# Performance work log

Hardware: AMD Instinct MI355X
Metric: run time of the kernel (lower is better)

## Reference

```python
import jax, jax.numpy as jnp
import numpy as np

B, C, H, W = 8, 256, 64, 64
R = 8
CP = max(C // R, 3)  # C' = 32


def setup_inputs() -> dict:
    key = jax.random.key(0)
    ks = jax.random.split(key, 9)
    s_in = 1.0 / np.sqrt(C)
    s_cp = 1.0 / np.sqrt(CP)
    return {
        "x": jax.random.normal(ks[0], (B, C, H, W), dtype=jnp.float32),
        "Wq": jax.random.uniform(ks[1], (CP, C), minval=-s_in, maxval=s_in, dtype=jnp.float32),
        "bq": jax.random.uniform(ks[2], (CP,), minval=-s_in, maxval=s_in, dtype=jnp.float32),
        "Wk": jax.random.uniform(ks[3], (CP, C), minval=-s_in, maxval=s_in, dtype=jnp.float32),
        "bk": jax.random.uniform(ks[4], (CP,), minval=-s_in, maxval=s_in, dtype=jnp.float32),
        "Wv": jax.random.uniform(ks[5], (CP, C), minval=-s_in, maxval=s_in, dtype=jnp.float32),
        "bv": jax.random.uniform(ks[6], (CP,), minval=-s_in, maxval=s_in, dtype=jnp.float32),
        "Wb": jax.random.uniform(ks[7], (C, CP), minval=-s_cp, maxval=s_cp, dtype=jnp.float32),
        "bb": jax.random.uniform(ks[8], (C,), minval=-s_cp, maxval=s_cp, dtype=jnp.float32),
    }


def reference(x, Wq, bq, Wk, bk, Wv, bv, Wb, bb):
    b, c, h, w = x.shape
    n = h * w
    xf = x.reshape(b, c, n)  # [B, C, N]
    # 1x1 convs == channel-wise linear projections
    q = jnp.einsum('oc,bcn->bon', Wq, xf) + bq[None, :, None]  # [B, C', N]
    k = jnp.einsum('oc,bcn->bon', Wk, xf) + bk[None, :, None]
    v = jnp.einsum('oc,bcn->bon', Wv, xf) + bv[None, :, None]
    # attention: softmax(Q^T K) over last dim -> [B, N, N]
    attn = jax.nn.softmax(jnp.einsum('bon,bom->bnm', q, k), axis=-1)
    # out[b,c,i] = sum_j v[b,c,j] * attn[b,j,i]
    out = jnp.einsum('bcj,bji->bci', v, attn)  # [B, C', N]
    back = jnp.einsum('co,bon->bcn', Wb, out) + bb[None, :, None]  # [B, C, N]
    return back.reshape(b, c, h, w) + x
```

## Files before the change

kernel.cpp:

```cpp
#include <hip/hip_runtime.h>
#include <hip/hip_bf16.h>

#define NB 8
#define CC 256
#define CP 32
#define NN 4096

typedef __attribute__((ext_vector_type(8))) short short8;
typedef __attribute__((ext_vector_type(4))) float floatx4;
typedef __attribute__((ext_vector_type(4))) int intx4;

static __device__ __forceinline__ ushort bf16r(float f) {
    __hip_bfloat16 h = __float2bfloat16(f);
    return *reinterpret_cast<ushort*>(&h);
}
static __device__ __forceinline__ float bf2f(ushort u) {
    union { unsigned int i; float f; } x;
    x.i = ((unsigned int)u) << 16;
    return x.f;
}
static __device__ __forceinline__ short8 load_frag(const ushort* p) {
    intx4 v = *reinterpret_cast<const intx4*>(p);
    return *reinterpret_cast<short8*>(&v);
}
static __device__ __forceinline__ unsigned int pk2(float a, float b) {
    unsigned int ua = __float_as_uint(a) + 0x8000u;
    unsigned int ub = __float_as_uint(b) + 0x8000u;
    return (ua >> 16) | (ub & 0xFFFF0000u);
}

__global__ void prep_w(const float* __restrict__ Wq, const float* __restrict__ Wk,
                       const float* __restrict__ Wv, ushort* __restrict__ W96) {
    int r = blockIdx.x, c = threadIdx.x;
    const float* src = (r < 32) ? (Wq + r * CC) : ((r < 64) ? (Wk + (r - 32) * CC) : (Wv + (r - 64) * CC));
    W96[r * CC + c] = bf16r(src[c]);
}

__global__ __launch_bounds__(256) void proj_kernel(
    const float* __restrict__ x, const ushort* __restrict__ W96,
    const float* __restrict__ bq, const float* __restrict__ bk, const float* __restrict__ bv,
    ushort* __restrict__ Qt, ushort* __restrict__ Kt, ushort* __restrict__ Vt) {
    int b = blockIdx.x >> 6;
    int nt = blockIdx.x & 63;
    int w = threadIdx.x >> 6, lane = threadIdx.x & 63;
    int l15 = lane & 15, q = lane >> 4;
    int n = nt * 64 + w * 16 + l15;
    const float* xb = x + (size_t)b * CC * NN + n;

    floatx4 acc[6];
#pragma unroll
    for (int t = 0; t < 6; t++) acc[t] = (floatx4){0.f, 0.f, 0.f, 0.f};

#pragma unroll
    for (int ks = 0; ks < 8; ks++) {
        int cbase = ks * 32 + q * 8;
        float xv[8];
#pragma unroll
        for (int jj = 0; jj < 8; jj++) xv[jj] = xb[(size_t)(cbase + jj) * NN];
        short8 bfrag;
#pragma unroll
        for (int jj = 0; jj < 8; jj++) bfrag[jj] = (short)bf16r(xv[jj]);
#pragma unroll
        for (int ot = 0; ot < 6; ot++) {
            short8 afrag = load_frag(&W96[(size_t)(ot * 16 + l15) * CC + ks * 32 + q * 8]);
            acc[ot] = __builtin_amdgcn_mfma_f32_16x16x32_bf16(afrag, bfrag, acc[ot], 0, 0, 0);
        }
    }
#pragma unroll
    for (int ot = 0; ot < 6; ot++) {
        const float* bias = (ot < 2) ? bq : ((ot < 4) ? bk : bv);
        ushort* dst = (ot < 2) ? Qt : ((ot < 4) ? Kt : Vt);
        int o0 = (ot & 1) * 16 + q * 4;
        float4 b4 = *reinterpret_cast<const float4*>(bias + o0);
        ushort4 pk;
        pk.x = bf16r(acc[ot][0] + b4.x);
        pk.y = bf16r(acc[ot][1] + b4.y);
        pk.z = bf16r(acc[ot][2] + b4.z);
        pk.w = bf16r(acc[ot][3] + b4.w);
        *reinterpret_cast<ushort4*>(&dst[((size_t)b * NN + n) * CP + o0]) = pk;
    }
}

__global__ __launch_bounds__(256) void passA_kernel(
    const ushort* __restrict__ Qt, const ushort* __restrict__ Kt, float* __restrict__ Fp) {
    __shared__ ushort kst[256 * CP];
    int bid = blockIdx.x;
    int mq = bid & 3;
    int jt = (bid >> 2) & 63;
    int b = bid >> 8;
    int w = threadIdx.x >> 6, lane = threadIdx.x & 63;
    int l15 = lane & 15, q = lane >> 4;
    int j = jt * 64 + w * 16 + l15;

    short8 af = load_frag(&Qt[((size_t)b * NN + j) * CP + q * 8]);
    floatx4 lacc = (floatx4){0.f, 0.f, 0.f, 0.f};

    for (int mc = 0; mc < 4; mc++) {
        int m0 = mq * 1024 + mc * 256;
        __syncthreads();
        {
            const intx4* src = reinterpret_cast<const intx4*>(&Kt[((size_t)b * NN + m0) * CP]);
            intx4* dst = reinterpret_cast<intx4*>(kst);
#pragma unroll
            for (int s = 0; s < 4; s++) dst[threadIdx.x + 256 * s] = src[threadIdx.x + 256 * s];
        }
        __syncthreads();
#pragma unroll
        for (int ms = 0; ms < 16; ms++) {
            short8 bf = load_frag(&kst[(ms * 16 + l15) * CP + q * 8]);
            floatx4 z = (floatx4){0.f, 0.f, 0.f, 0.f};
            floatx4 s = __builtin_amdgcn_mfma_f32_16x16x32_bf16(af, bf, z, 0, 0, 0);
            lacc[0] += __expf(s[0]);
            lacc[1] += __expf(s[1]);
            lacc[2] += __expf(s[2]);
            lacc[3] += __expf(s[3]);
        }
    }
#pragma unroll
    for (int d = 1; d < 16; d <<= 1) {
        lacc[0] += __shfl_xor(lacc[0], d, 64);
        lacc[1] += __shfl_xor(lacc[1], d, 64);
        lacc[2] += __shfl_xor(lacc[2], d, 64);
        lacc[3] += __shfl_xor(lacc[3], d, 64);
    }
    if (l15 == 0) {
        float4 f4;
        f4.x = lacc[0];
        f4.y = lacc[1];
        f4.z = lacc[2];
        f4.w = lacc[3];
        *reinterpret_cast<float4*>(&Fp[((size_t)mq * NB + b) * NN + jt * 64 + w * 16 + q * 4]) = f4;
    }
}

__global__ __launch_bounds__(256) void fold_kernel(
    const ushort* __restrict__ Vt, const float* __restrict__ Fp, ushort* __restrict__ Vp) {
    __shared__ ushort tile[32][264];
    const size_t PL = (size_t)NB * NN;
    int b = blockIdx.x >> 4, nt = blockIdx.x & 15;
    int t = threadIdx.x;
    int n = nt * 256 + t;
    size_t bn = (size_t)b * NN + n;
    float f = 1.0f / (Fp[bn] + Fp[PL + bn] + Fp[2 * PL + bn] + Fp[3 * PL + bn]);
    const ushort* src = &Vt[bn * CP];
#pragma unroll
    for (int c8 = 0; c8 < 4; c8++) {
        intx4 raw = *reinterpret_cast<const intx4*>(src + c8 * 8);
        const ushort* us = reinterpret_cast<const ushort*>(&raw);
#pragma unroll
        for (int e = 0; e < 8; e++) {
            tile[c8 * 8 + e][t] = bf16r(bf2f(us[e]) * f);
        }
    }
    __syncthreads();
#pragma unroll
    for (int c = 0; c < 32; c++) {
        Vp[((size_t)b * CP + c) * NN + nt * 256 + t] = tile[c][t];
    }
}

__global__ __launch_bounds__(256) void passB_kernel(
    const ushort* __restrict__ Qt, const ushort* __restrict__ Kt, const ushort* __restrict__ Vp,
    const float* __restrict__ x, const float* __restrict__ Wb, const float* __restrict__ bb,
    float* __restrict__ out) {
    __shared__ ushort qst[256 * CP];
    __shared__ ushort vst[32 * 264];

    int b = blockIdx.x >> 6, it = blockIdx.x & 63;
    int w = threadIdx.x >> 6, lane = threadIdx.x & 63;
    int l15 = lane & 15, q = lane >> 4;
    int iw = w & 1, jp = w >> 1;
    int i0 = it * 64 + iw * 32;

    short8 kf0 = load_frag(&Kt[((size_t)b * NN + i0 + l15) * CP + q * 8]);
    short8 kf1 = load_frag(&Kt[((size_t)b * NN + i0 + 16 + l15) * CP + q * 8]);

    floatx4 acc00 = (floatx4){0.f, 0.f, 0.f, 0.f};
    floatx4 acc10 = (floatx4){0.f, 0.f, 0.f, 0.f};
    floatx4 acc01 = (floatx4){0.f, 0.f, 0.f, 0.f};
    floatx4 acc11 = (floatx4){0.f, 0.f, 0.f, 0.f};

    int qoff = (((l15 >> 2) * 8 + (l15 & 3)) * CP) + q * 8;
    int voff0 = l15 * 264 + q * 8;
    int voff1 = (16 + l15) * 264 + q * 8;

    for (int j0 = 0; j0 < NN; j0 += 256) {
        __syncthreads();
        {
            const intx4* qsrc = reinterpret_cast<const intx4*>(&Qt[((size_t)b * NN + j0) * CP]);
            intx4* qdst = reinterpret_cast<intx4*>(qst);
#pragma unroll
            for (int s = 0; s < 4; s++) qdst[threadIdx.x + 256 * s] = qsrc[threadIdx.x + 256 * s];
            int r = threadIdx.x >> 3, ci = threadIdx.x & 7;
            const intx4* vsrc = reinterpret_cast<const intx4*>(&Vp[((size_t)b * CP + r) * NN + j0]);
            intx4* vdst = reinterpret_cast<intx4*>(&vst[r * 264]);
#pragma unroll
            for (int s = 0; s < 4; s++) vdst[ci + 8 * s] = vsrc[ci + 8 * s];
        }
        __syncthreads();
#pragma unroll
        for (int jss = 0; jss < 4; jss++) {
            int jl = (jss * 2 + jp) * 32;
            short8 a0 = load_frag(&qst[jl * CP + qoff]);
            short8 a1 = load_frag(&qst[jl * CP + qoff + 4 * CP]);
            floatx4 z = (floatx4){0.f, 0.f, 0.f, 0.f};
            floatx4 s0A = __builtin_amdgcn_mfma_f32_16x16x32_bf16(a0, kf0, z, 0, 0, 0);
            floatx4 s1A = __builtin_amdgcn_mfma_f32_16x16x32_bf16(a1, kf0, z, 0, 0, 0);
            floatx4 s0B = __builtin_amdgcn_mfma_f32_16x16x32_bf16(a0, kf1, z, 0, 0, 0);
            floatx4 s1B = __builtin_amdgcn_mfma_f32_16x16x32_bf16(a1, kf1, z, 0, 0, 0);

            union { intx4 v; short8 s; } wa, wb2;
            wa.v.x = pk2(__expf(s0A[0]), __expf(s0A[1]));
            wa.v.y = pk2(__expf(s0A[2]), __expf(s0A[3]));
            wa.v.z = pk2(__expf(s1A[0]), __expf(s1A[1]));
            wa.v.w = pk2(__expf(s1A[2]), __expf(s1A[3]));
            wb2.v.x = pk2(__expf(s0B[0]), __expf(s0B[1]));
            wb2.v.y = pk2(__expf(s0B[2]), __expf(s0B[3]));
            wb2.v.z = pk2(__expf(s1B[0]), __expf(s1B[1]));
            wb2.v.w = pk2(__expf(s1B[2]), __expf(s1B[3]));

            short8 va0 = load_frag(&vst[voff0 + jl]);
            short8 va1 = load_frag(&vst[voff1 + jl]);
            acc00 = __builtin_amdgcn_mfma_f32_16x16x32_bf16(va0, wa.s, acc00, 0, 0, 0);
            acc10 = __builtin_amdgcn_mfma_f32_16x16x32_bf16(va1, wa.s, acc10, 0, 0, 0);
            acc01 = __builtin_amdgcn_mfma_f32_16x16x32_bf16(va0, wb2.s, acc01, 0, 0, 0);
            acc11 = __builtin_amdgcn_mfma_f32_16x16x32_bf16(va1, wb2.s, acc11, 0, 0, 0);
        }
    }

    __syncthreads();
    float (*olds)[68] = reinterpret_cast<float(*)[68]>(qst);
    if (jp == 0) {
#pragma unroll
        for (int r = 0; r < 4; r++) {
            olds[q * 4 + r][iw * 32 + l15] = acc00[r];
            olds[16 + q * 4 + r][iw * 32 + l15] = acc10[r];
            olds[q * 4 + r][iw * 32 + 16 + l15] = acc01[r];
            olds[16 + q * 4 + r][iw * 32 + 16 + l15] = acc11[r];
        }
    }
    __syncthreads();
    if (jp == 1) {
#pragma unroll
        for (int r = 0; r < 4; r++) {
            olds[q * 4 + r][iw * 32 + l15] += acc00[r];
            olds[16 + q * 4 + r][iw * 32 + l15] += acc10[r];
            olds[q * 4 + r][iw * 32 + 16 + l15] += acc01[r];
            olds[16 + q * 4 + r][iw * 32 + 16 + l15] += acc11[r];
        }
    }
    __syncthreads();

    int t = threadIdx.x;
    int i4 = (t & 15) * 4;
    int cb = t >> 4;
    float4 accv[16];
#pragma unroll
    for (int cc = 0; cc < 16; cc++) {
        float bbv = bb[cb + 16 * cc];
        accv[cc].x = bbv; accv[cc].y = bbv; accv[cc].z = bbv; accv[cc].w = bbv;
    }
#pragma unroll 4
    for (int o = 0; o < 32; o++) {
        float4 ovv = *reinterpret_cast<const float4*>(&olds[o][i4]);
#pragma unroll
        for (int cc = 0; cc < 16; cc++) {
            float wv = Wb[(size_t)(cb + 16 * cc) * CP + o];
            accv[cc].x += wv * ovv.x;
            accv[cc].y += wv * ovv.y;
            accv[cc].z += wv * ovv.z;
            accv[cc].w += wv * ovv.w;
        }
    }
    size_t xbase = (size_t)b * CC * NN + (size_t)it * 64 + i4;
#pragma unroll
    for (int cc = 0; cc < 16; cc++) {
        int cout = cb + 16 * cc;
        float4 xv = *reinterpret_cast<const float4*>(&x[xbase + (size_t)cout * NN]);
        float4 res;
        res.x = accv[cc].x + xv.x;
        res.y = accv[cc].y + xv.y;
        res.z = accv[cc].z + xv.z;
        res.w = accv[cc].w + xv.w;
        *reinterpret_cast<float4*>(&out[xbase + (size_t)cout * NN]) = res;
    }
}

extern "C" void kernel_launch(void* const* d_in, const int* in_sizes, int n_in,
                              void* d_out, int out_size, void* d_ws, size_t ws_size,
                              hipStream_t stream) {
    const float* x  = (const float*)d_in[0];
    const float* Wq = (const float*)d_in[1];
    const float* bq = (const float*)d_in[2];
    const float* Wk = (const float*)d_in[3];
    const float* bk = (const float*)d_in[4];
    const float* Wv = (const float*)d_in[5];
    const float* bv = (const float*)d_in[6];
    const float* Wb = (const float*)d_in[7];
    const float* bb = (const float*)d_in[8];
    float* out = (float*)d_out;

    char* ws = (char*)d_ws;
    ushort* Qt  = (ushort*)(ws);
    ushort* Kt  = (ushort*)(ws + (2u << 20));
    ushort* Vt  = (ushort*)(ws + (4u << 20));
    ushort* Vp  = (ushort*)(ws + (6u << 20));
    float*  Fp  = (float*) (ws + (8u << 20));
    ushort* W96 = (ushort*)(ws + (8u << 20) + (1u << 19));

    prep_w<<<96, 256, 0, stream>>>(Wq, Wk, Wv, W96);
    proj_kernel<<<512, 256, 0, stream>>>(x, W96, bq, bk, bv, Qt, Kt, Vt);
    passA_kernel<<<2048, 256, 0, stream>>>(Qt, Kt, Fp);
    fold_kernel<<<128, 256, 0, stream>>>(Vt, Fp, Vp);
    passB_kernel<<<512, 256, 0, stream>>>(Qt, Kt, Vp, x, Wb, bb, out);
}
```

Measured before the change: 202.8 us.

## Fold log2e into Q, pad LDS, MFMA back-projection, retile passB and proj

Pre-scales Wq and bq by log2(e) so the softmax exponentials can use the native exp2. K and Q tiles in LDS are padded to 40 elements per row to reduce bank conflicts. The projection kernel now stages x through LDS with coalesced float4 loads. passB gets half-width i-tiles, four-way j splitting and twice as many blocks, and its final Wb projection becomes a bf16 MFMA. fold_kernel is also retiled. Occupancy hints are added, at the cost of some extra bf16 rounding in the output projection.

```diff
diff --git a/kernel.cpp b/kernel.cpp
--- a/kernel.cpp
+++ b/kernel.cpp
@@ -5,6 +5,7 @@
 #define CC 256
 #define CP 32
 #define NN 4096
+#define LOG2E 1.44269504088896340736f
 
 typedef __attribute__((ext_vector_type(8))) short short8;
 typedef __attribute__((ext_vector_type(4))) float floatx4;
@@ -28,66 +29,100 @@
     unsigned int ub = __float_as_uint(b) + 0x8000u;
     return (ua >> 16) | (ub & 0xFFFF0000u);
 }
+static __device__ __forceinline__ ushort pk1(float a) {
+    return (ushort)((__float_as_uint(a) + 0x8000u) >> 16);
+}
+static __device__ __forceinline__ float fexp2(float x) {
+#if defined(__has_builtin)
+#if __has_builtin(__builtin_amdgcn_exp2f)
+    return __builtin_amdgcn_exp2f(x);
+#else
+    return __expf(x * 0.69314718055994530942f);
+#endif
+#else
+    return __expf(x * 0.69314718055994530942f);
+#endif
+}
 
 __global__ void prep_w(const float* __restrict__ Wq, const float* __restrict__ Wk,
-                       const float* __restrict__ Wv, ushort* __restrict__ W96) {
+                       const float* __restrict__ Wv, const float* __restrict__ Wb,
+                       ushort* __restrict__ W96, ushort* __restrict__ W2b) {
     int r = blockIdx.x, c = threadIdx.x;
-    const float* src = (r < 32) ? (Wq + r * CC) : ((r < 64) ? (Wk + (r - 32) * CC) : (Wv + (r - 64) * CC));
-    W96[r * CC + c] = bf16r(src[c]);
+    if (r < 96) {
+        const float* src = (r < 32) ? (Wq + r * CC) : ((r < 64) ? (Wk + (r - 32) * CC) : (Wv + (r - 64) * CC));
+        float scale = (r < 32) ? LOG2E : 1.0f;
+        W96[r * CC + c] = bf16r(src[c] * scale);
+    } else {
+        int idx = (r - 96) * 256 + c;
+        W2b[idx] = bf16r(Wb[idx]);
+    }
 }
 
 __global__ __launch_bounds__(256) void proj_kernel(
     const float* __restrict__ x, const ushort* __restrict__ W96,
     const float* __restrict__ bq, const float* __restrict__ bk, const float* __restrict__ bv,
     ushort* __restrict__ Qt, ushort* __restrict__ Kt, ushort* __restrict__ Vt) {
-    int b = blockIdx.x >> 6;
-    int nt = blockIdx.x & 63;
-    int w = threadIdx.x >> 6, lane = threadIdx.x & 63;
-    int l15 = lane & 15, q = lane >> 4;
-    int n = nt * 64 + w * 16 + l15;
-    const float* xb = x + (size_t)b * CC * NN + n;
-
+    __shared__ ushort xt[64 * 264];
+    int b = blockIdx.x >> 6, nt = blockIdx.x & 63;
+    int t = threadIdx.x;
+    int n0 = nt * 64;
+    {
+        int cq = t >> 4, n4 = (t & 15) * 4;
+#pragma unroll
+        for (int cc = 0; cc < 4; cc++) {
+            int c_base = cc * 64 + cq * 4;
+            float4 xv[4];
+#pragma unroll
+            for (int e = 0; e < 4; e++)
+                xv[e] = *reinterpret_cast<const float4*>(&x[((size_t)b * CC + c_base + e) * NN + n0 + n4]);
+            const float* xs = reinterpret_cast<const float*>(xv);
+#pragma unroll
+            for (int jj = 0; jj < 4; jj++) {
+                ushort4 u;
+                u.x = pk1(xs[0 * 4 + jj]);
+                u.y = pk1(xs[1 * 4 + jj]);
+                u.z = pk1(xs[2 * 4 + jj]);
+                u.w = pk1(xs[3 * 4 + jj]);
+                *reinterpret_cast<ushort4*>(&xt[(n4 + jj) * 264 + c_base]) = u;
+            }
+        }
+    }
+    __syncthreads();
+    int w = t >> 6, lane = t & 63, l15 = lane & 15, q = lane >> 4;
     floatx4 acc[6];
 #pragma unroll
-    for (int t = 0; t < 6; t++) acc[t] = (floatx4){0.f, 0.f, 0.f, 0.f};
-
+    for (int k = 0; k < 6; k++) acc[k] = (floatx4){0.f, 0.f, 0.f, 0.f};
 #pragma unroll
     for (int ks = 0; ks < 8; ks++) {
-        int cbase = ks * 32 + q * 8;
-        float xv[8];
-#pragma unroll
-        for (int jj = 0; jj < 8; jj++) xv[jj] = xb[(size_t)(cbase + jj) * NN];
-        short8 bfrag;
-#pragma unroll
-        for (int jj = 0; jj < 8; jj++) bfrag[jj] = (short)bf16r(xv[jj]);
+        short8 bfrag = load_frag(&xt[(w * 16 + l15) * 264 + ks * 32 + q * 8]);
 #pragma unroll
         for (int ot = 0; ot < 6; ot++) {
             short8 afrag = load_frag(&W96[(size_t)(ot * 16 + l15) * CC + ks * 32 + q * 8]);
             acc[ot] = __builtin_amdgcn_mfma_f32_16x16x32_bf16(afrag, bfrag, acc[ot], 0, 0, 0);
         }
     }
+    int n = n0 + w * 16 + l15;
 #pragma unroll
     for (int ot = 0; ot < 6; ot++) {
         const float* bias = (ot < 2) ? bq : ((ot < 4) ? bk : bv);
         ushort* dst = (ot < 2) ? Qt : ((ot < 4) ? Kt : Vt);
         int o0 = (ot & 1) * 16 + q * 4;
         float4 b4 = *reinterpret_cast<const float4*>(bias + o0);
+        float sc = (ot < 2) ? LOG2E : 1.0f;
         ushort4 pk;
-        pk.x = bf16r(acc[ot][0] + b4.x);
-        pk.y = bf16r(acc[ot][1] + b4.y);
-        pk.z = bf16r(acc[ot][2] + b4.z);
-        pk.w = bf16r(acc[ot][3] + b4.w);
+        pk.x = bf16r(acc[ot][0] + b4.x * sc);
+        pk.y = bf16r(acc[ot][1] + b4.y * sc);
+        pk.z = bf16r(acc[ot][2] + b4.z * sc);
+        pk.w = bf16r(acc[ot][3] + b4.w * sc);
         *reinterpret_cast<ushort4*>(&dst[((size_t)b * NN + n) * CP + o0]) = pk;
     }
 }
 
-__global__ __launch_bounds__(256) void passA_kernel(
+__global__ __launch_bounds__(256, 4) void passA_kernel(
     const ushort* __restrict__ Qt, const ushort* __restrict__ Kt, float* __restrict__ Fp) {
-    __shared__ ushort kst[256 * CP];
+    __shared__ ushort kst[256 * 40];
     int bid = blockIdx.x;
-    int mq = bid & 3;
-    int jt = (bid >> 2) & 63;
-    int b = bid >> 8;
+    int mq = bid & 3, jt = (bid >> 2) & 63, b = bid >> 8;
     int w = threadIdx.x >> 6, lane = threadIdx.x & 63;
     int l15 = lane & 15, q = lane >> 4;
     int j = jt * 64 + w * 16 + l15;
@@ -102,18 +137,21 @@
             const intx4* src = reinterpret_cast<const intx4*>(&Kt[((size_t)b * NN + m0) * CP]);
             intx4* dst = reinterpret_cast<intx4*>(kst);
 #pragma unroll
-            for (int s = 0; s < 4; s++) dst[threadIdx.x + 256 * s] = src[threadIdx.x + 256 * s];
+            for (int s = 0; s < 4; s++) {
+                int g = threadIdx.x + 256 * s;
+                dst[(g >> 2) * 5 + (g & 3)] = src[g];
+            }
         }
         __syncthreads();
 #pragma unroll
         for (int ms = 0; ms < 16; ms++) {
-            short8 bf = load_frag(&kst[(ms * 16 + l15) * CP + q * 8]);
+            short8 bf = load_frag(&kst[(ms * 16 + l15) * 40 + q * 8]);
             floatx4 z = (floatx4){0.f, 0.f, 0.f, 0.f};
             floatx4 s = __builtin_amdgcn_mfma_f32_16x16x32_bf16(af, bf, z, 0, 0, 0);
-            lacc[0] += __expf(s[0]);
-            lacc[1] += __expf(s[1]);
-            lacc[2] += __expf(s[2]);
-            lacc[3] += __expf(s[3]);
+            lacc[0] += fexp2(s[0]);
+            lacc[1] += fexp2(s[1]);
+            lacc[2] += fexp2(s[2]);
+            lacc[3] += fexp2(s[3]);
         }
     }
 #pragma unroll
@@ -125,52 +163,52 @@
     }
     if (l15 == 0) {
         float4 f4;
-        f4.x = lacc[0];
-        f4.y = lacc[1];
-        f4.z = lacc[2];
-        f4.w = lacc[3];
+        f4.x = lacc[0]; f4.y = lacc[1]; f4.z = lacc[2]; f4.w = lacc[3];
         *reinterpret_cast<float4*>(&Fp[((size_t)mq * NB + b) * NN + jt * 64 + w * 16 + q * 4]) = f4;
     }
 }
 
 __global__ __launch_bounds__(256) void fold_kernel(
     const ushort* __restrict__ Vt, const float* __restrict__ Fp, ushort* __restrict__ Vp) {
-    __shared__ ushort tile[32][264];
+    __shared__ ushort tile[32 * 136];
     const size_t PL = (size_t)NB * NN;
-    int b = blockIdx.x >> 4, nt = blockIdx.x & 15;
+    int b = blockIdx.x >> 5, nc = blockIdx.x & 31;
     int t = threadIdx.x;
-    int n = nt * 256 + t;
+    int half = t >> 7, nl = t & 127;
+    int n = nc * 128 + nl;
     size_t bn = (size_t)b * NN + n;
     float f = 1.0f / (Fp[bn] + Fp[PL + bn] + Fp[2 * PL + bn] + Fp[3 * PL + bn]);
-    const ushort* src = &Vt[bn * CP];
-#pragma unroll
-    for (int c8 = 0; c8 < 4; c8++) {
-        intx4 raw = *reinterpret_cast<const intx4*>(src + c8 * 8);
+    const ushort* src = &Vt[bn * CP + half * 16];
+#pragma unroll
+    for (int g = 0; g < 2; g++) {
+        intx4 raw = *reinterpret_cast<const intx4*>(src + g * 8);
         const ushort* us = reinterpret_cast<const ushort*>(&raw);
 #pragma unroll
         for (int e = 0; e < 8; e++) {
-            tile[c8 * 8 + e][t] = bf16r(bf2f(us[e]) * f);
+            tile[(half * 16 + g * 8 + e) * 136 + nl] = pk1(bf2f(us[e]) * f);
         }
     }
     __syncthreads();
 #pragma unroll
-    for (int c = 0; c < 32; c++) {
-        Vp[((size_t)b * CP + c) * NN + nt * 256 + t] = tile[c][t];
-    }
-}
-
-__global__ __launch_bounds__(256) void passB_kernel(
+    for (int cc = 0; cc < 16; cc++) {
+        int c = half * 16 + cc;
+        Vp[((size_t)b * CP + c) * NN + nc * 128 + nl] = tile[c * 136 + nl];
+    }
+}
+
+__global__ __launch_bounds__(256, 4) void passB_kernel(
     const ushort* __restrict__ Qt, const ushort* __restrict__ Kt, const ushort* __restrict__ Vp,
-    const float* __restrict__ x, const float* __restrict__ Wb, const float* __restrict__ bb,
+    const ushort* __restrict__ W2b, const float* __restrict__ bb, const float* __restrict__ x,
     float* __restrict__ out) {
-    __shared__ ushort qst[256 * CP];
+    __shared__ ushort qst[256 * 40];
     __shared__ ushort vst[32 * 264];
 
-    int b = blockIdx.x >> 6, it = blockIdx.x & 63;
+    int bid = blockIdx.x;
+    int it = bid & 127, b = bid >> 7;
     int w = threadIdx.x >> 6, lane = threadIdx.x & 63;
     int l15 = lane & 15, q = lane >> 4;
-    int iw = w & 1, jp = w >> 1;
-    int i0 = it * 64 + iw * 32;
+    int jp = w;
+    int i0 = it * 32;
 
     short8 kf0 = load_frag(&Kt[((size_t)b * NN + i0 + l15) * CP + q * 8]);
     short8 kf1 = load_frag(&Kt[((size_t)b * NN + i0 + 16 + l15) * CP + q * 8]);
@@ -180,17 +218,19 @@
     floatx4 acc01 = (floatx4){0.f, 0.f, 0.f, 0.f};
     floatx4 acc11 = (floatx4){0.f, 0.f, 0.f, 0.f};
 
-    int qoff = (((l15 >> 2) * 8 + (l15 & 3)) * CP) + q * 8;
-    int voff0 = l15 * 264 + q * 8;
-    int voff1 = (16 + l15) * 264 + q * 8;
-
-    for (int j0 = 0; j0 < NN; j0 += 256) {
+    int qrow = (l15 >> 2) * 8 + (l15 & 3);
+
+    for (int jc = 0; jc < 16; jc++) {
+        int j0 = jc * 256;
         __syncthreads();
         {
             const intx4* qsrc = reinterpret_cast<const intx4*>(&Qt[((size_t)b * NN + j0) * CP]);
             intx4* qdst = reinterpret_cast<intx4*>(qst);
 #pragma unroll
-            for (int s = 0; s < 4; s++) qdst[threadIdx.x + 256 * s] = qsrc[threadIdx.x + 256 * s];
+            for (int s = 0; s < 4; s++) {
+                int g = threadIdx.x + 256 * s;
+                qdst[(g >> 2) * 5 + (g & 3)] = qsrc[g];
+            }
             int r = threadIdx.x >> 3, ci = threadIdx.x & 7;
             const intx4* vsrc = reinterpret_cast<const intx4*>(&Vp[((size_t)b * CP + r) * NN + j0]);
             intx4* vdst = reinterpret_cast<intx4*>(&vst[r * 264]);
@@ -199,10 +239,12 @@
         }
         __syncthreads();
 #pragma unroll
-        for (int jss = 0; jss < 4; jss++) {
-            int jl = (jss * 2 + jp) * 32;
-            short8 a0 = load_frag(&qst[jl * CP + qoff]);
-            short8 a1 = load_frag(&qst[jl * CP + qoff + 4 * CP]);
+        for (int ss = 0; ss < 2; ss++) {
+            int jl = (ss * 4 + jp) * 32;
+            short8 va0 = load_frag(&vst[l15 * 264 + jl + q * 8]);
+            short8 va1 = load_frag(&vst[(16 + l15) * 264 + jl + q * 8]);
+            short8 a0 = load_frag(&qst[(jl + qrow) * 40 + q * 8]);
+            short8 a1 = load_frag(&qst[(jl + qrow + 4) * 40 + q * 8]);
             floatx4 z = (floatx4){0.f, 0.f, 0.f, 0.f};
             floatx4 s0A = __builtin_amdgcn_mfma_f32_16x16x32_bf16(a0, kf0, z, 0, 0, 0);
             floatx4 s1A = __builtin_amdgcn_mfma_f32_16x16x32_bf16(a1, kf0, z, 0, 0, 0);
@@ -210,17 +252,15 @@
             floatx4 s1B = __builtin_amdgcn_mfma_f32_16x16x32_bf16(a1, kf1, z, 0, 0, 0);
 
             union { intx4 v; short8 s; } wa, wb2;
-            wa.v.x = pk2(__expf(s0A[0]), __expf(s0A[1]));
-            wa.v.y = pk2(__expf(s0A[2]), __expf(s0A[3]));
-            wa.v.z = pk2(__expf(s1A[0]), __expf(s1A[1]));
-            wa.v.w = pk2(__expf(s1A[2]), __expf(s1A[3]));
-            wb2.v.x = pk2(__expf(s0B[0]), __expf(s0B[1]));
-            wb2.v.y = pk2(__expf(s0B[2]), __expf(s0B[3]));
-            wb2.v.z = pk2(__expf(s1B[0]), __expf(s1B[1]));
-            wb2.v.w = pk2(__expf(s1B[2]), __expf(s1B[3]));
-
-            short8 va0 = load_frag(&vst[voff0 + jl]);
-            short8 va1 = load_frag(&vst[voff1 + jl]);
+            wa.v.x = pk2(fexp2(s0A[0]), fexp2(s0A[1]));
+            wa.v.y = pk2(fexp2(s0A[2]), fexp2(s0A[3]));
+            wa.v.z = pk2(fexp2(s1A[0]), fexp2(s1A[1]));
+            wa.v.w = pk2(fexp2(s1A[2]), fexp2(s1A[3]));
+            wb2.v.x = pk2(fexp2(s0B[0]), fexp2(s0B[1]));
+            wb2.v.y = pk2(fexp2(s0B[2]), fexp2(s0B[3]));
+            wb2.v.z = pk2(fexp2(s1B[0]), fexp2(s1B[1]));
+            wb2.v.w = pk2(fexp2(s1B[2]), fexp2(s1B[3]));
+
             acc00 = __builtin_amdgcn_mfma_f32_16x16x32_bf16(va0, wa.s, acc00, 0, 0, 0);
             acc10 = __builtin_amdgcn_mfma_f32_16x16x32_bf16(va1, wa.s, acc10, 0, 0, 0);
             acc01 = __builtin_amdgcn_mfma_f32_16x16x32_bf16(va0, wb2.s, acc01, 0, 0, 0);
@@ -229,60 +269,50 @@
     }
 
     __syncthreads();
-    float (*olds)[68] = reinterpret_cast<float(*)[68]>(qst);
-    if (jp == 0) {
-#pragma unroll
-        for (int r = 0; r < 4; r++) {
-            olds[q * 4 + r][iw * 32 + l15] = acc00[r];
-            olds[16 + q * 4 + r][iw * 32 + l15] = acc10[r];
-            olds[q * 4 + r][iw * 32 + 16 + l15] = acc01[r];
-            olds[16 + q * 4 + r][iw * 32 + 16 + l15] = acc11[r];
-        }
+    float* olds4 = reinterpret_cast<float*>(qst);
+    int mbase = jp * (32 * 33);
+#pragma unroll
+    for (int r = 0; r < 4; r++) {
+        olds4[mbase + (q * 4 + r) * 33 + l15] = acc00[r];
+        olds4[mbase + (16 + q * 4 + r) * 33 + l15] = acc10[r];
+        olds4[mbase + (q * 4 + r) * 33 + 16 + l15] = acc01[r];
+        olds4[mbase + (16 + q * 4 + r) * 33 + 16 + l15] = acc11[r];
     }
     __syncthreads();
-    if (jp == 1) {
-#pragma unroll
-        for (int r = 0; r < 4; r++) {
-            olds[q * 4 + r][iw * 32 + l15] += acc00[r];
-            olds[16 + q * 4 + r][iw * 32 + l15] += acc10[r];
-            olds[q * 4 + r][iw * 32 + 16 + l15] += acc01[r];
-            olds[16 + q * 4 + r][iw * 32 + 16 + l15] += acc11[r];
-        }
-    }
-    __syncthreads();
-
-    int t = threadIdx.x;
-    int i4 = (t & 15) * 4;
-    int cb = t >> 4;
-    float4 accv[16];
-#pragma unroll
-    for (int cc = 0; cc < 16; cc++) {
-        float bbv = bb[cb + 16 * cc];
-        accv[cc].x = bbv; accv[cc].y = bbv; accv[cc].z = bbv; accv[cc].w = bbv;
-    }
-#pragma unroll 4
-    for (int o = 0; o < 32; o++) {
-        float4 ovv = *reinterpret_cast<const float4*>(&olds[o][i4]);
-#pragma unroll
-        for (int cc = 0; cc < 16; cc++) {
-            float wv = Wb[(size_t)(cb + 16 * cc) * CP + o];
-            accv[cc].x += wv * ovv.x;
-            accv[cc].y += wv * ovv.y;
-            accv[cc].z += wv * ovv.z;
-            accv[cc].w += wv * ovv.w;
-        }
-    }
-    size_t xbase = (size_t)b * CC * NN + (size_t)it * 64 + i4;
-#pragma unroll
-    for (int cc = 0; cc < 16; cc++) {
-        int cout = cb + 16 * cc;
-        float4 xv = *reinterpret_cast<const float4*>(&x[xbase + (size_t)cout * NN]);
-        float4 res;
-        res.x = accv[cc].x + xv.x;
-        res.y = accv[cc].y + xv.y;
-        res.z = accv[cc].z + xv.z;
-        res.w = accv[cc].w + xv.w;
-        *reinterpret_cast<float4*>(&out[xbase + (size_t)cout * NN]) = res;
+
+    short8 bfr[2];
+#pragma unroll
+    for (int s = 0; s < 2; s++) {
+        float o8[8];
+#pragma unroll
+        for (int jj = 0; jj < 8; jj++) {
+            int o = q * 8 + jj;
+            int idx = o * 33 + s * 16 + l15;
+            o8[jj] = olds4[idx] + olds4[1056 + idx] + olds4[2112 + idx] + olds4[3168 + idx];
+        }
+        union { intx4 v; short8 sh; } u;
+        u.v.x = pk2(o8[0], o8[1]);
+        u.v.y = pk2(o8[2], o8[3]);
+        u.v.z = pk2(o8[4], o8[5]);
+        u.v.w = pk2(o8[6], o8[7]);
+        bfr[s] = u.sh;
+    }
+    int c0 = w * 64;
+#pragma unroll
+    for (int cs = 0; cs < 4; cs++) {
+        short8 af = load_frag(&W2b[(size_t)(c0 + cs * 16 + l15) * CP + q * 8]);
+#pragma unroll
+        for (int s = 0; s < 2; s++) {
+            floatx4 z = (floatx4){0.f, 0.f, 0.f, 0.f};
+            floatx4 d = __builtin_amdgcn_mfma_f32_16x16x32_bf16(af, bfr[s], z, 0, 0, 0);
+#pragma unroll
+            for (int r = 0; r < 4; r++) {
+                int c = c0 + cs * 16 + q * 4 + r;
+                int i = i0 + s * 16 + l15;
+                size_t idx = ((size_t)b * CC + c) * NN + i;
+                out[idx] = d[r] + bb[c] + x[idx];
+            }
+        }
     }
 }
 
@@ -303,14 +333,15 @@
     char* ws = (char*)d_ws;
     ushort* Qt  = (ushort*)(ws);
     ushort* Kt  = (ushort*)(ws + (2u << 20));
-    ushort* Vt  = (ushort*)(ws + (4u << 20));
-    ushort* Vp  = (ushort*)(ws + (6u << 20));
+    ushort* Vp  = (ushort*)(ws + (4u << 20));
+    ushort* Vt  = (ushort*)(ws + (6u << 20));
     float*  Fp  = (float*) (ws + (8u << 20));
     ushort* W96 = (ushort*)(ws + (8u << 20) + (1u << 19));
-
-    prep_w<<<96, 256, 0, stream>>>(Wq, Wk, Wv, W96);
+    ushort* W2b = (ushort*)(ws + (8u << 20) + (1u << 19) + (48u << 10));
+
+    prep_w<<<128, 256, 0, stream>>>(Wq, Wk, Wv, Wb, W96, W2b);
     proj_kernel<<<512, 256, 0, stream>>>(x, W96, bq, bk, bv, Qt, Kt, Vt);
     passA_kernel<<<2048, 256, 0, stream>>>(Qt, Kt, Fp);
-    fold_kernel<<<128, 256, 0, stream>>>(Vt, Fp, Vp);
-    passB_kernel<<<512, 256, 0, stream>>>(Qt, Kt, Vp, x, Wb, bb, out);
-}
+    fold_kernel<<<256, 256, 0, stream>>>(Vt, Fp, Vp);
+    passB_kernel<<<1024, 256, 0, stream>>>(Qt, Kt, Vp, W2b, bb, x, out);
+}
```

Result: faster. 164.7 us (-18.8%).
